# Kernel optimization log

Measured on AMD Instinct MI355X. Metric: run time of the kernel, lower is better.

The kernel has to match this reference:

```python
import jax, jax.numpy as jnp
import numpy as np

T = 65536  # number of frames

# Precomputed strict upper-triangle index pairs (matches htriu/ptriu/ltriu masks:
# dist+1 >= 1 > 0 everywhere, so boolean_mask((dist+1)*triu != 0) followed by -1
# is exactly 'take dist at strict upper-triangle entries').
_HIU = np.triu_indices(21, k=1)  # 210 pairs
_PIU = np.triu_indices(25, k=1)  # 300 pairs
_LIU = np.triu_indices(20, k=1)  # 190 pairs


def _triu_dist(pts, iu):
    # pts: (T, N, C); returns (T, P) pairwise Euclidean distances at i<j pairs
    d = pts[:, iu[0], :] - pts[:, iu[1], :]
    return jnp.sqrt(jnp.sum(d * d, axis=-1))


def setup_inputs() -> dict:
    key = jax.random.key(0)
    x = jax.random.normal(key, (T, 115, 3), dtype=jnp.float32)
    return {"x": x}


def reference(x):
    # NaN -> 0
    x = jnp.where(jnp.isnan(x), jnp.float32(0.0), x)
    lefth = x[:, 40:61, :]   # (T, 21, 3)
    righth = x[:, 94:115, :] # (T, 21, 3)
    pose = x[:, 61:86, :]    # (T, 25, 3)
    lip = x[:, :40, :]       # (T, 40, 3)

    # pick the dominant hand (global scalar condition)
    lefth_sum = jnp.sum((lefth != 0).astype(jnp.float32))
    righth_sum = jnp.sum((righth != 0).astype(jnp.float32))
    cond = lefth_sum > righth_sum

    h_x = jnp.where(cond, lefth, righth)  # (T, 21, 3)
    xfeat = jnp.where(cond,
                      jnp.concatenate([lefth, pose, lip], axis=1),
                      jnp.concatenate([righth, pose, lip], axis=1))  # (T, 86, 3)

    # mirror x-coordinate for left hand
    xc = jnp.where(cond, -xfeat[:, :, 0], xfeat[:, :, 0])
    xfeat = jnp.concatenate([xc[:, :, None], xfeat[:, :, 1:]], axis=-1)

    # frame compaction: drop frames whose hand is all-zero.
    # Implemented as a stable sort of the keep mask (kept frames first, order
    # preserved) so shapes stay static; with randn inputs every frame is kept
    # and this is exactly tf.boolean_mask.
    keep = jnp.sum(h_x.reshape(-1, 21 * 3), axis=1) != 0
    order = jnp.argsort(jnp.logical_not(keep), stable=True)
    xfeat = xfeat[order]

    # temporal deltas, zero-padded at the end
    dxyz = jnp.concatenate(
        [xfeat[:-1] - xfeat[1:], jnp.zeros((1, 86, 3), dtype=xfeat.dtype)], axis=0)

    hdist = _triu_dist(xfeat[:, :21, :3], _HIU)     # (T, 210) hand pairwise
    pdist = _triu_dist(xfeat[:, 21:46, :2], _PIU)   # (T, 300) pose pairwise (xy)
    oldist = _triu_dist(xfeat[:, 46:66, :2], _LIU)  # (T, 190) outer lip (xy)
    ildist = _triu_dist(xfeat[:, 66:86, :2], _LIU)  # (T, 190) inner lip (xy)

    out = jnp.concatenate([
        xfeat[:, :21, :3].reshape(-1, 21 * 3),
        xfeat[:, 21:46, :2].reshape(-1, 25 * 2),
        xfeat[:, 46:66, :2].reshape(-1, 20 * 2),
        dxyz[:, :21, :3].reshape(-1, 21 * 3),
        dxyz[:, 21:46, :2].reshape(-1, 25 * 2),
        dxyz[:, 46:66, :2].reshape(-1, 20 * 2),
        hdist, pdist, oldist, ildist,
    ], axis=-1)  # (T, 1196)

    out = out[:100]
    return out.reshape(1, -1, 1196)
```

## Files before the change

kernel.cpp:

```cpp
#include <hip/hip_runtime.h>
#include <hip/hip_bf16.h>
#include <math.h>

#define T_FRAMES 65536
#define FSTRIDE  345

__device__ __forceinline__ void triu_ab(int l, int N, int& a, int& b) {
  int a0 = 0, rem = l, row = N - 1;
  while (rem >= row) { rem -= row; ++a0; --row; }
  a = a0; b = a0 + 1 + rem;
}

__global__ __launch_bounds__(256) void phase1(const float* __restrict__ x,
                                              uchar2* __restrict__ keepF) {
  const int wave = threadIdx.x >> 6;
  const int lane = threadIdx.x & 63;
  const int f = (blockIdx.x << 2) + wave;
  const float* xf = x + (size_t)f * FSTRIDE;
  float vl = 0.f, vr = 0.f; int cl = 0, cr = 0;
  if (lane < 63) {
    float a = xf[120 + lane]; if (isnan(a)) a = 0.f;
    float b = xf[282 + lane]; if (isnan(b)) b = 0.f;
    vl = a; vr = b; cl = (a != 0.f); cr = (b != 0.f);
  }
  for (int off = 32; off > 0; off >>= 1) {
    vl += __shfl_down(vl, off, 64);
    vr += __shfl_down(vr, off, 64);
    cl += __shfl_down(cl, off, 64);
    cr += __shfl_down(cr, off, 64);
  }
  if (lane == 0) {
    uchar2 k;
    k.x = (unsigned char)(cl | ((vl != 0.f) ? 0x80 : 0));
    k.y = (unsigned char)(cr | ((vr != 0.f) ? 0x80 : 0));
    keepF[f] = k;
  }
}

__global__ __launch_bounds__(1024) void phase2(const uchar2* __restrict__ keepF,
                                               int* __restrict__ condP,
                                               int* __restrict__ order) {
  const int tid  = threadIdx.x;
  const int lane = tid & 63;
  const int wave = tid >> 6;
  __shared__ int sL[16], sR[16];
  __shared__ unsigned long long sM[16];
  __shared__ int sBase, sCond;

  const uint4* kp = (const uint4*)keepF;
  int cl = 0, cr = 0;
  for (int i = tid; i < (T_FRAMES * 2 / 16); i += 1024) {
    uint4 v = kp[i];
    unsigned t;
    t = v.x & 0x7F7F7F7Fu; cl += (t & 0xFF) + ((t >> 16) & 0xFF); cr += ((t >> 8) & 0xFF) + ((t >> 24) & 0xFF);
    t = v.y & 0x7F7F7F7Fu; cl += (t & 0xFF) + ((t >> 16) & 0xFF); cr += ((t >> 8) & 0xFF) + ((t >> 24) & 0xFF);
    t = v.z & 0x7F7F7F7Fu; cl += (t & 0xFF) + ((t >> 16) & 0xFF); cr += ((t >> 8) & 0xFF) + ((t >> 24) & 0xFF);
    t = v.w & 0x7F7F7F7Fu; cl += (t & 0xFF) + ((t >> 16) & 0xFF); cr += ((t >> 8) & 0xFF) + ((t >> 24) & 0xFF);
  }
  for (int off = 32; off > 0; off >>= 1) {
    cl += __shfl_down(cl, off, 64);
    cr += __shfl_down(cr, off, 64);
  }
  if (lane == 0) { sL[wave] = cl; sR[wave] = cr; }
  __syncthreads();
  if (tid == 0) {
    int L = 0, R = 0;
    for (int i = 0; i < 16; ++i) { L += sL[i]; R += sR[i]; }
    sCond = (L > R) ? 1 : 0;
    condP[0] = sCond;
    sBase = 0;
  }
  __syncthreads();
  const int cond = sCond;

  for (int pass = 0; pass < 2; ++pass) {
    for (int base = 0; base < T_FRAMES; base += 1024) {
      if (sBase >= 101) break;
      uchar2 k = keepF[base + tid];
      int flag = ((cond ? (int)k.x : (int)k.y) >> 7) & 1;
      if (pass) flag ^= 1;
      unsigned long long m = __ballot(flag);
      if (lane == 0) sM[wave] = m;
      __syncthreads();
      int pos = sBase;
      for (int w = 0; w < wave; ++w) pos += __popcll(sM[w]);
      pos += (int)__popcll(m & ((1ull << lane) - 1ull));
      if (flag && pos < 101) order[pos] = base + tid;
      __syncthreads();
      if (tid == 0) {
        int tot = 0;
        for (int w = 0; w < 16; ++w) tot += (int)__popcll(sM[w]);
        sBase += tot;
      }
      __syncthreads();
    }
  }
}

__global__ __launch_bounds__(256) void phase3(const float* __restrict__ x,
                                              const int* __restrict__ condP,
                                              const int* __restrict__ order,
                                              float* __restrict__ out) {
  __shared__ float A[258], B[258];
  const int row  = blockIdx.x;
  const int cond = condP[0];
  const int f = order[row], g = order[row + 1];
  const float* xf = x + (size_t)f * FSTRIDE;
  const float* xg = x + (size_t)g * FSTRIDE;

  for (int idx = threadIdx.x; idx < 258; idx += blockDim.x) {
    const int p = idx / 3, c = idx - p * 3;
    const int s = (p < 21) ? (cond ? 40 + p : 94 + p) : ((p < 46) ? p + 40 : p - 46);
    float va = xf[s * 3 + c]; if (isnan(va)) va = 0.f;
    float vb = xg[s * 3 + c]; if (isnan(vb)) vb = 0.f;
    if (cond && c == 0) { va = -va; vb = -vb; }
    A[idx] = va; B[idx] = vb;
  }
  __syncthreads();

  float* o = out + (size_t)row * 1196;
  for (int j = threadIdx.x; j < 1196; j += blockDim.x) {
    float v;
    if (j < 306) {
      int jj = j; bool diff = false;
      if (jj >= 153) { diff = true; jj -= 153; }
      int p, c;
      if (jj < 63)       { p = jj / 3;             c = jj - p * 3; }
      else if (jj < 113) { int t = jj - 63;  p = 21 + (t >> 1); c = t & 1; }
      else               { int t = jj - 113; p = 46 + (t >> 1); c = t & 1; }
      v = A[p * 3 + c];
      if (diff) v -= B[p * 3 + c];
    } else if (j < 516) {
      int a, b; triu_ab(j - 306, 21, a, b);
      const float dx = A[a*3]   - A[b*3];
      const float dy = A[a*3+1] - A[b*3+1];
      const float dz = A[a*3+2] - A[b*3+2];
      v = sqrtf(dx*dx + dy*dy + dz*dz);
    } else if (j < 816) {
      int a, b; triu_ab(j - 516, 25, a, b);
      a += 21; b += 21;
      const float dx = A[a*3] - A[b*3], dy = A[a*3+1] - A[b*3+1];
      v = sqrtf(dx*dx + dy*dy);
    } else if (j < 1006) {
      int a, b; triu_ab(j - 816, 20, a, b);
      a += 46; b += 46;
      const float dx = A[a*3] - A[b*3], dy = A[a*3+1] - A[b*3+1];
      v = sqrtf(dx*dx + dy*dy);
    } else {
      int a, b; triu_ab(j - 1006, 20, a, b);
      a += 66; b += 66;
      const float dx = A[a*3] - A[b*3], dy = A[a*3+1] - A[b*3+1];
      v = sqrtf(dx*dx + dy*dy);
    }
    o[j] = v;
  }
}

extern "C" void kernel_launch(void* const* d_in, const int* in_sizes, int n_in,
                              void* d_out, int out_size, void* d_ws, size_t ws_size,
                              hipStream_t stream) {
  const float* x = (const float*)d_in[0];
  float* out = (float*)d_out;
  char* ws = (char*)d_ws;
  int*    condP = (int*)ws;
  int*    order = (int*)(ws + 16);
  uchar2* keepF = (uchar2*)(ws + 512);

  phase1<<<T_FRAMES / 4, 256, 0, stream>>>(x, keepF);
  phase2<<<1, 1024, 0, stream>>>(keepF, condP, order);
  phase3<<<100, 256, 0, stream>>>(x, condP, order, out);
}
```

Before: 135.3 us.

## Pack per-frame keep flags into bitmasks and pre-reduce hand counts in phase1

```diff
diff --git a/kernel.cpp b/kernel.cpp
--- a/kernel.cpp
+++ b/kernel.cpp
@@ -1,9 +1,10 @@
 #include <hip/hip_runtime.h>
-#include <hip/hip_bf16.h>
 #include <math.h>
 
 #define T_FRAMES 65536
 #define FSTRIDE  345
+#define ROWB     4784
+
 
 __device__ __forceinline__ void triu_ab(int l, int N, int& a, int& b) {
   int a0 = 0, rem = l, row = N - 1;
@@ -12,51 +13,66 @@
 }
 
 __global__ __launch_bounds__(256) void phase1(const float* __restrict__ x,
-                                              uchar2* __restrict__ keepF) {
+                                              ushort* __restrict__ keepbits,
+                                              int2* __restrict__ partials) {
   const int wave = threadIdx.x >> 6;
   const int lane = threadIdx.x & 63;
-  const int f = (blockIdx.x << 2) + wave;
-  const float* xf = x + (size_t)f * FSTRIDE;
-  float vl = 0.f, vr = 0.f; int cl = 0, cr = 0;
-  if (lane < 63) {
-    float a = xf[120 + lane]; if (isnan(a)) a = 0.f;
-    float b = xf[282 + lane]; if (isnan(b)) b = 0.f;
-    vl = a; vr = b; cl = (a != 0.f); cr = (b != 0.f);
+  const int w = (blockIdx.x << 2) + wave;
+  const float* xw = x + (size_t)w * 8 * FSTRIDE;
+
+  int cl = 0, cr = 0;
+  unsigned bits = 0;
+  for (int i = 0; i < 8; ++i) {
+    const float* xf = xw + i * FSTRIDE;
+    float a = 0.f, b = 0.f;
+    if (lane < 63) {
+      a = xf[120 + lane]; if (isnan(a)) a = 0.f;
+      b = xf[282 + lane]; if (isnan(b)) b = 0.f;
+    }
+    cl += (a != 0.f);
+    cr += (b != 0.f);
+    float va = a, vb = b;
+    for (int off = 32; off > 0; off >>= 1) {
+      va += __shfl_down(va, off, 64);
+      vb += __shfl_down(vb, off, 64);
+    }
+    if (lane == 0)
+      bits |= (((va != 0.f) ? 1u : 0u) << (2 * i)) |
+              (((vb != 0.f) ? 1u : 0u) << (2 * i + 1));
   }
   for (int off = 32; off > 0; off >>= 1) {
-    vl += __shfl_down(vl, off, 64);
-    vr += __shfl_down(vr, off, 64);
     cl += __shfl_down(cl, off, 64);
     cr += __shfl_down(cr, off, 64);
   }
+  __shared__ int bL[4], bR[4];
   if (lane == 0) {
-    uchar2 k;
-    k.x = (unsigned char)(cl | ((vl != 0.f) ? 0x80 : 0));
-    k.y = (unsigned char)(cr | ((vr != 0.f) ? 0x80 : 0));
-    keepF[f] = k;
+    keepbits[w] = (ushort)bits;
+    bL[wave] = cl; bR[wave] = cr;
   }
+  __syncthreads();
+  if (threadIdx.x == 0)
+    partials[blockIdx.x] = make_int2(bL[0] + bL[1] + bL[2] + bL[3],
+                                     bR[0] + bR[1] + bR[2] + bR[3]);
 }
 
-__global__ __launch_bounds__(1024) void phase2(const uchar2* __restrict__ keepF,
-                                               int* __restrict__ condP,
-                                               int* __restrict__ order) {
+__global__ __launch_bounds__(1024) void phase2(const uint4* __restrict__ kb,
+                                               const int4* __restrict__ pp,
+                                               char* __restrict__ outB) {
   const int tid  = threadIdx.x;
   const int lane = tid & 63;
   const int wave = tid >> 6;
+  __shared__ unsigned int sKeep[4096];
   __shared__ int sL[16], sR[16];
   __shared__ unsigned long long sM[16];
+  __shared__ int sOrder[104];
   __shared__ int sBase, sCond;
 
-  const uint4* kp = (const uint4*)keepF;
-  int cl = 0, cr = 0;
-  for (int i = tid; i < (T_FRAMES * 2 / 16); i += 1024) {
-    uint4 v = kp[i];
-    unsigned t;
-    t = v.x & 0x7F7F7F7Fu; cl += (t & 0xFF) + ((t >> 16) & 0xFF); cr += ((t >> 8) & 0xFF) + ((t >> 24) & 0xFF);
-    t = v.y & 0x7F7F7F7Fu; cl += (t & 0xFF) + ((t >> 16) & 0xFF); cr += ((t >> 8) & 0xFF) + ((t >> 24) & 0xFF);
-    t = v.z & 0x7F7F7F7Fu; cl += (t & 0xFF) + ((t >> 16) & 0xFF); cr += ((t >> 8) & 0xFF) + ((t >> 24) & 0xFF);
-    t = v.w & 0x7F7F7F7Fu; cl += (t & 0xFF) + ((t >> 16) & 0xFF); cr += ((t >> 8) & 0xFF) + ((t >> 24) & 0xFF);
-  }
+  uint4 v = kb[tid];
+  sKeep[tid * 4 + 0] = v.x; sKeep[tid * 4 + 1] = v.y;
+  sKeep[tid * 4 + 2] = v.z; sKeep[tid * 4 + 3] = v.w;
+
+  int4 p = pp[tid];
+  int cl = p.x + p.z, cr = p.y + p.w;
   for (int off = 32; off > 0; off >>= 1) {
     cl += __shfl_down(cl, off, 64);
     cr += __shfl_down(cr, off, 64);
@@ -67,44 +83,51 @@
     int L = 0, R = 0;
     for (int i = 0; i < 16; ++i) { L += sL[i]; R += sR[i]; }
     sCond = (L > R) ? 1 : 0;
-    condP[0] = sCond;
     sBase = 0;
   }
   __syncthreads();
   const int cond = sCond;
+  const int sel  = cond ? 0 : 1;
 
   for (int pass = 0; pass < 2; ++pass) {
     for (int base = 0; base < T_FRAMES; base += 1024) {
       if (sBase >= 101) break;
-      uchar2 k = keepF[base + tid];
-      int flag = ((cond ? (int)k.x : (int)k.y) >> 7) & 1;
+      const int f = base + tid;
+      const unsigned u = sKeep[f >> 4];
+      int flag = (int)((u >> (((f >> 3) & 1) * 16 + (f & 7) * 2 + sel)) & 1u);
       if (pass) flag ^= 1;
       unsigned long long m = __ballot(flag);
       if (lane == 0) sM[wave] = m;
       __syncthreads();
       int pos = sBase;
-      for (int w = 0; w < wave; ++w) pos += __popcll(sM[w]);
+      for (int w2 = 0; w2 < wave; ++w2) pos += (int)__popcll(sM[w2]);
       pos += (int)__popcll(m & ((1ull << lane) - 1ull));
-      if (flag && pos < 101) order[pos] = base + tid;
+      if (flag && pos < 101) sOrder[pos] = f;
       __syncthreads();
       if (tid == 0) {
         int tot = 0;
-        for (int w = 0; w < 16; ++w) tot += (int)__popcll(sM[w]);
+        for (int w2 = 0; w2 < 16; ++w2) tot += (int)__popcll(sM[w2]);
         sBase += tot;
       }
       __syncthreads();
     }
   }
+  __syncthreads();
+  if (tid < 100) {
+    int4 rec;
+    rec.x = cond; rec.y = sOrder[tid]; rec.z = sOrder[tid + 1]; rec.w = 0;
+    *(int4*)(outB + (size_t)tid * ROWB) = rec;
+  }
 }
 
 __global__ __launch_bounds__(256) void phase3(const float* __restrict__ x,
-                                              const int* __restrict__ condP,
-                                              const int* __restrict__ order,
                                               float* __restrict__ out) {
   __shared__ float A[258], B[258];
-  const int row  = blockIdx.x;
-  const int cond = condP[0];
-  const int f = order[row], g = order[row + 1];
+  const int row = blockIdx.x;
+  float* o = out + (size_t)row * 1196;
+  const int4 rec = *(const int4*)o;
+  const int cond = rec.x;
+  const int f = rec.y, g = rec.z;
   const float* xf = x + (size_t)f * FSTRIDE;
   const float* xg = x + (size_t)g * FSTRIDE;
 
@@ -118,7 +141,6 @@
   }
   __syncthreads();
 
-  float* o = out + (size_t)row * 1196;
   for (int j = threadIdx.x; j < 1196; j += blockDim.x) {
     float v;
     if (j < 306) {
@@ -159,14 +181,13 @@
 extern "C" void kernel_launch(void* const* d_in, const int* in_sizes, int n_in,
                               void* d_out, int out_size, void* d_ws, size_t ws_size,
                               hipStream_t stream) {
+  (void)in_sizes; (void)n_in; (void)out_size; (void)d_ws; (void)ws_size;
   const float* x = (const float*)d_in[0];
-  float* out = (float*)d_out;
-  char* ws = (char*)d_ws;
-  int*    condP = (int*)ws;
-  int*    order = (int*)(ws + 16);
-  uchar2* keepF = (uchar2*)(ws + 512);
+  char* ob = (char*)d_out;
+  ushort* keepbits = (ushort*)ob;
+  int2*   partials = (int2*)(ob + 16384);
 
-  phase1<<<T_FRAMES / 4, 256, 0, stream>>>(x, keepF);
-  phase2<<<1, 1024, 0, stream>>>(keepF, condP, order);
-  phase3<<<100, 256, 0, stream>>>(x, condP, order, out);
+  phase1<<<2048, 256, 0, stream>>>(x, keepbits, partials);
+  phase2<<<1, 1024, 0, stream>>>((const uint4*)ob, (const int4*)(ob + 16384), ob);
+  phase3<<<100, 256, 0, stream>>>(x, (float*)d_out);
 }
```

Measured after the change: 134.6 us. No clear change (-0.5%).
